# Performance work log

Hardware: AMD Instinct MI355X
Metric: run time of the kernel (lower is better)

Reference implementation:

```python
import jax, jax.numpy as jnp
import numpy as np

B, N, IN, HID, OUT, H = 8, 1024, 64, 64, 64, 4


def dense_gat(x, adj, W, a_src, a_dst, bias, heads):
    # x: [B,N,Fin], adj: [B,N,N] (0/1, self-loops already set), W: [heads*C, Fin]
    b, n, _ = x.shape
    c = W.shape[0] // heads
    h = (x @ W.T).reshape(b, n, heads, c)                      # [B,N,H,C]
    s = jnp.einsum('bnhc,hc->bnh', h, a_src)                   # source scores
    d = jnp.einsum('bnhc,hc->bnh', h, a_dst)                   # dest scores
    # alpha[b,i,j,h] = s[b,j,h] + d[b,i,h]
    alpha = s[:, None, :, :] + d[:, :, None, :]                # [B,N,N,H]
    alpha = jax.nn.leaky_relu(alpha, 0.2)
    alpha = jnp.where(adj[..., None] > 0, alpha, jnp.float32(-1e9))
    alpha = jax.nn.softmax(alpha, axis=2)                      # softmax over neighbors j
    out = jnp.einsum('bijh,bjhc->bihc', alpha, h)              # [B,N,H,C]
    return out.reshape(b, n, heads * c) + bias


def setup_inputs() -> dict:
    key = jax.random.key(0)
    ks = jax.random.split(key, 24)
    rn = lambda k, shape: (jax.random.normal(k, shape, jnp.float32) * 0.05)
    node_features = jax.random.normal(ks[0], (B, N, IN), jnp.float32)
    adj = jax.random.randint(ks[1], (B, N, N), 0, 2, jnp.int32)
    d = dict(
        node_features=node_features, adj=adj,
        w1=rn(ks[2], (H * HID, IN)),  as1=rn(ks[3], (H, HID)), ad1=rn(ks[4], (H, HID)), b1=rn(ks[5], (H * HID,)),
        w2=rn(ks[6], (H * HID, H * HID)), as2=rn(ks[7], (H, HID)), ad2=rn(ks[8], (H, HID)), b2=rn(ks[9], (H * HID,)),
        w3=rn(ks[10], (OUT, H * HID)), as3=rn(ks[11], (1, OUT)), ad3=rn(ks[12], (1, OUT)), b3=rn(ks[13], (OUT,)),
        wn=rn(ks[14], (OUT, OUT)), bn=rn(ks[15], (OUT,)),
        wg=rn(ks[16], (OUT, OUT)), bg=rn(ks[17], (OUT,)),
        wv=rn(ks[18], (1, 2 * OUT)), bv=rn(ks[19], (1,)),
    )
    return d


def reference(node_features, adj, w1, as1, ad1, b1, w2, as2, ad2, b2,
              w3, as3, ad3, b3, wn, bn, wg, bg, wv, bv):
    n = node_features.shape[1]
    adj_sl = jnp.maximum(adj, jnp.eye(n, dtype=adj.dtype)[None])  # add self-loops
    x = jax.nn.relu(dense_gat(node_features, adj_sl, w1, as1, ad1, b1, H))
    x = jax.nn.relu(dense_gat(x, adj_sl, w2, as2, ad2, b2, H))
    x = jax.nn.relu(dense_gat(x, adj_sl, w3, as3, ad3, b3, 1))     # [B,N,OUT]
    g = jnp.broadcast_to(x.sum(axis=-2, keepdims=True), x.shape)   # [B,N,OUT]
    h = jnp.concatenate([x @ wn.T + bn, g @ wg.T + bg], axis=-1)   # [B,N,2*OUT]
    h = jax.nn.relu(h)
    return (h @ wv.T + bv).squeeze(-1)                             # [B,N]
```

## Files before the change

kernel.cpp:

```cpp
#include <hip/hip_runtime.h>
#include <stdint.h>

#define NB 8
#define NN 1024
#define LOG2E 1.44269504088896f

typedef short short8 __attribute__((ext_vector_type(8)));
typedef float floatx4 __attribute__((ext_vector_type(4)));

static __device__ __forceinline__ short f2bf(float x) {
    union { float f; uint32_t u; } v; v.f = x;
    uint32_t r = (v.u + 0x7fffu + ((v.u >> 16) & 1u)) >> 16;
    return (short)r;
}

__global__ __launch_bounds__(256) void prep_all(const int* __restrict__ adj,
        uint64_t* __restrict__ am,
        const float* __restrict__ x0, const float* __restrict__ w1,
        const float* __restrict__ w2, const float* __restrict__ w3,
        const float* __restrict__ wn,
        ushort* __restrict__ x0b, ushort* __restrict__ wb1,
        ushort* __restrict__ wb2, ushort* __restrict__ wb3,
        ushort* __restrict__ wnb, float* __restrict__ gsum) {
    if (blockIdx.x < 2048) {
        int wave = blockIdx.x * 4 + (threadIdx.x >> 6);
        int lane = threadIdx.x & 63;
        int b = wave >> 10;
        int i = wave & 1023;
        const int* row = adj + ((size_t)b * NN + i) * NN;
        uint64_t* outp = am + ((size_t)b * NN + i) * 16;
        for (int it = 0; it < 16; ++it) {
            int j = it * 64 + lane;
            int v = (row[j] > 0) || (j == i);
            uint64_t m = __ballot(v);
            if (lane == 0) outp[it] = m;
        }
        return;
    }
    int idx = (blockIdx.x - 2048) * 256 + threadIdx.x;
    const float* src; ushort* dst; int li;
    if (idx < 131072)      { src = x0; dst = x0b; li = idx; }
    else if (idx < 135168) { src = w1; dst = wb1; li = idx - 131072; }
    else if (idx < 151552) { src = w2; dst = wb2; li = idx - 135168; }
    else if (idx < 155648) { src = w3; dst = wb3; li = idx - 151552; }
    else if (idx < 156672) { src = wn; dst = wnb; li = idx - 155648; }
    else if (idx < 156800) {
        ((float4*)gsum)[idx - 156672] = make_float4(0.f, 0.f, 0.f, 0.f);
        return;
    } else return;
    float4 v = ((const float4*)src)[li];
    ushort4 o;
    o.x = (ushort)f2bf(v.x); o.y = (ushort)f2bf(v.y);
    o.z = (ushort)f2bf(v.z); o.w = (ushort)f2bf(v.w);
    ((ushort4*)dst)[li] = o;
}

template<int K>
__global__ __launch_bounds__(256, 4) void gemm_mfma(const ushort* __restrict__ X,
        const ushort* __restrict__ Wt, ushort* __restrict__ hbT,
        const float* __restrict__ asrc, const float* __restrict__ adst,
        float* __restrict__ s_t, float* __restrict__ d_t, int nheads) {
    __shared__ ushort smem[2][64][88];
    int m0 = blockIdx.x * 64, n0 = blockIdx.y * 64;
    int hd = blockIdx.y;
    int tid = threadIdx.x, w = tid >> 6, L = tid & 63;
    int m15 = L & 15, kq = L >> 4;
    floatx4 acc[4];
#pragma unroll
    for (int ct = 0; ct < 4; ++ct) acc[ct] = (floatx4){0.f, 0.f, 0.f, 0.f};

    for (int k0 = 0; k0 < K; k0 += 64) {
#pragma unroll
        for (int it = 0; it < 2; ++it) {
            int idx = tid + it * 256;
            int r = idx >> 3, sg = idx & 7;
            *(uint4*)&smem[0][r][sg * 8] = *(const uint4*)&X[(size_t)(m0 + r) * K + k0 + sg * 8];
            *(uint4*)&smem[1][r][sg * 8] = *(const uint4*)&Wt[(size_t)(n0 + r) * K + k0 + sg * 8];
        }
        __syncthreads();
#pragma unroll
        for (int ks = 0; ks < 2; ++ks) {
            short8 a = *(const short8*)&smem[0][16 * w + m15][ks * 32 + kq * 8];
#pragma unroll
            for (int ct = 0; ct < 4; ++ct) {
                short8 bfr = *(const short8*)&smem[1][ct * 16 + m15][ks * 32 + kq * 8];
                acc[ct] = __builtin_amdgcn_mfma_f32_16x16x32_bf16(a, bfr, acc[ct], 0, 0, 0);
            }
        }
        __syncthreads();
    }

    float asv[4], adv[4];
#pragma unroll
    for (int ct = 0; ct < 4; ++ct) {
        asv[ct] = asrc[hd * 64 + ct * 16 + m15];
        adv[ct] = adst[hd * 64 + ct * 16 + m15];
    }
#pragma unroll
    for (int r = 0; r < 4; ++r) {
        float sp = acc[0][r] * asv[0] + acc[1][r] * asv[1] + acc[2][r] * asv[2] + acc[3][r] * asv[3];
        float dp = acc[0][r] * adv[0] + acc[1][r] * adv[1] + acc[2][r] * adv[2] + acc[3][r] * adv[3];
#pragma unroll
        for (int off = 1; off < 16; off <<= 1) {
            sp += __shfl_xor(sp, off);
            dp += __shfl_xor(dp, off);
        }
        if (m15 == 0) {
            int mg = m0 + 16 * w + kq * 4 + r;
            int bb = mg >> 10, node = mg & 1023;
            s_t[((size_t)(bb * nheads + hd)) * NN + node] = sp;
            d_t[((size_t)(bb * nheads + hd)) * NN + node] = dp;
        }
    }

    ushort* tb = (ushort*)smem;
#pragma unroll
    for (int ct = 0; ct < 4; ++ct)
#pragma unroll
        for (int r = 0; r < 4; ++r)
            tb[(ct * 16 + m15) * 80 + 16 * w + kq * 4 + r] = (ushort)f2bf(acc[ct][r]);
    __syncthreads();
    int bb = m0 >> 10, node0 = m0 & 1023;
    size_t base = ((size_t)(bb * nheads + hd) * 64) * NN + node0;
    int c = tid >> 2, s2 = (tid & 3) * 2;
#pragma unroll
    for (int e = 0; e < 2; ++e) {
        int sg = s2 + e;
        *(uint4*)&hbT[base + (size_t)c * NN + sg * 8] = *(const uint4*)&tb[c * 80 + sg * 8];
    }
}

__global__ __launch_bounds__(256, 4) void gat_agg_mfma(
        const ushort* __restrict__ hbT, const uint64_t* __restrict__ am,
        const float* __restrict__ s_t, const float* __restrict__ d_t,
        const float* __restrict__ bias, ushort* __restrict__ Xb,
        float* __restrict__ gsum, int nheads, int do_colsum) {
    __shared__ float s_lds[NN];
    __shared__ float d_lds[32];
    __shared__ float li_lds[32];
    __shared__ float red4[4];
    __shared__ float lsum_part[32];
    __shared__ uint64_t adj_lds[16][32];
    __shared__ ushort hb[2][64][88];

    int i0 = blockIdx.x * 32;
    int hd = blockIdx.y;
    int b  = blockIdx.z;
    int HC = nheads * 64;
    int tid = threadIdx.x, w = tid >> 6, L = tid & 63;
    int m15 = L & 15, kq = L >> 4;
    int p = w >> 1, q = w & 1;
    int tp = tid & 127;

    const float* srow = s_t + ((size_t)b * nheads + hd) * NN;
    const float* drow = d_t + ((size_t)b * nheads + hd) * NN;
    float lm = -1e30f;
    for (int j = tid; j < NN; j += 256) {
        float v = srow[j];
        s_lds[j] = v;
        lm = fmaxf(lm, v);
    }
#pragma unroll
    for (int off = 32; off; off >>= 1) lm = fmaxf(lm, __shfl_xor(lm, off));
    if (L == 0) red4[w] = lm;
    if (tid < 32) d_lds[tid] = drow[i0 + tid];
#pragma unroll
    for (int it = 0; it < 2; ++it) {
        int idx = tid + it * 256;
        int r = idx >> 4, wd = idx & 15;
        adj_lds[wd][r] = am[((size_t)b * NN + i0 + r) * 16 + wd];
    }
    __syncthreads();

    float smax = fmaxf(fmaxf(red4[0], red4[1]), fmaxf(red4[2], red4[3]));
    float d_i = d_lds[16 * q + m15];
    float m_up = smax + d_i;
    m_up = m_up > 0.f ? m_up : 0.2f * m_up;
    float m2n = -m_up * LOG2E;

    floatx4 acc[4];
#pragma unroll
    for (int ct = 0; ct < 4; ++ct) acc[ct] = (floatx4){0.f, 0.f, 0.f, 0.f};
    float lsum = 0.f;

    const ushort* hbase = hbT + ((size_t)(b * nheads + hd) * 64) * NN;

    for (int t = 0; t < 8; ++t) {
        int jc = p * 8 + t;
#pragma unroll
        for (int it = 0; it < 4; ++it) {
            int idx = tp + it * 128;
            int c = idx >> 3, sg = idx & 7;
            *(uint4*)&hb[p][c][sg * 8] = *(const uint4*)&hbase[(size_t)c * NN + jc * 64 + sg * 8];
        }
        __syncthreads();

        uint64_t word = adj_lds[jc][16 * q + m15];
#pragma unroll
        for (int ks = 0; ks < 2; ++ks) {
            int jb = jc * 64 + ks * 32 + kq * 8;
            float sv[8];
            *(float4*)&sv[0] = *(const float4*)&s_lds[jb];
            *(float4*)&sv[4] = *(const float4*)&s_lds[jb + 4];
            unsigned byte = (unsigned)((word >> (ks * 32 + kq * 8)) & 0xffull);
            short8 afrag;
#pragma unroll
            for (int u = 0; u < 8; ++u) {
                float sc = sv[u] + d_i;
                float lk = fmaxf(sc, 0.2f * sc);
#if __has_builtin(__builtin_amdgcn_exp2f)
                float arg = __builtin_fmaf(lk, LOG2E, m2n);
                arg = ((byte >> u) & 1u) ? arg : -1e30f;
                float e = __builtin_amdgcn_exp2f(arg);
#else
                float e = __expf(lk - m_up);
                e = ((byte >> u) & 1u) ? e : 0.f;
#endif
                lsum += e;
                ((ushort*)&afrag)[u] = (ushort)(__float_as_uint(e) >> 16);
            }
#pragma unroll
            for (int ct = 0; ct < 4; ++ct) {
                short8 bfr = *(const short8*)&hb[p][ct * 16 + m15][ks * 32 + kq * 8];
                acc[ct] = __builtin_amdgcn_mfma_f32_16x16x32_bf16(afrag, bfr, acc[ct], 0, 0, 0);
            }
        }
        __syncthreads();
    }

    lsum += __shfl_xor(lsum, 16);
    lsum += __shfl_xor(lsum, 32);

    float* accbuf = (float*)&hb[0][0][0];
    if (p == 1) {
#pragma unroll
        for (int ct = 0; ct < 4; ++ct)
#pragma unroll
            for (int r = 0; r < 4; ++r)
                accbuf[(16 * q + kq * 4 + r) * 66 + ct * 16 + m15] = acc[ct][r];
        if (kq == 0) lsum_part[16 * q + m15] = lsum;
    }
    __syncthreads();
    if (p == 0) {
#pragma unroll
        for (int ct = 0; ct < 4; ++ct)
#pragma unroll
            for (int r = 0; r < 4; ++r)
                acc[ct][r] += accbuf[(16 * q + kq * 4 + r) * 66 + ct * 16 + m15];
        float ltot = lsum + lsum_part[16 * q + m15];
        if (kq == 0) li_lds[16 * q + m15] = 1.f / ltot;
    }
    __syncthreads();

    if (p == 0) {
        float bv4[4];
#pragma unroll
        for (int ct = 0; ct < 4; ++ct) bv4[ct] = bias[hd * 64 + ct * 16 + m15];
#pragma unroll
        for (int ct = 0; ct < 4; ++ct) {
            float cs = 0.f;
#pragma unroll
            for (int r = 0; r < 4; ++r) {
                int row = 16 * q + kq * 4 + r;
                float v = acc[ct][r] * li_lds[row] + bv4[ct];
                v = fmaxf(v, 0.f);
                cs += v;
                size_t off = ((size_t)(b * NN + i0 + row)) * HC + hd * 64 + ct * 16 + m15;
                Xb[off] = (ushort)f2bf(v);
            }
            if (do_colsum) {
                cs += __shfl_xor(cs, 16);
                cs += __shfl_xor(cs, 32);
                if (kq == 0) atomicAdd(&gsum[b * 64 + ct * 16 + m15], cs);
            }
        }
    }
}

__global__ __launch_bounds__(256) void readout_fused(
        const ushort* __restrict__ xb, const ushort* __restrict__ wnb,
        const float* __restrict__ bn, const float* __restrict__ wg,
        const float* __restrict__ bg, const float* __restrict__ wv,
        const float* __restrict__ bv, const float* __restrict__ gsum,
        float* __restrict__ outp) {
    __shared__ ushort xs[64][88];
    __shared__ ushort wns[64][88];
    __shared__ float gcs;
    int b = blockIdx.y, n0 = blockIdx.x * 64;
    int tid = threadIdx.x, w = tid >> 6, L = tid & 63;
    int m15 = L & 15, kq = L >> 4;
#pragma unroll
    for (int it = 0; it < 2; ++it) {
        int idx = tid + it * 256;
        int r = idx >> 3, sg = idx & 7;
        *(uint4*)&xs[r][sg * 8]  = *(const uint4*)&xb[(size_t)(b * NN + n0 + r) * 64 + sg * 8];
        *(uint4*)&wns[r][sg * 8] = *(const uint4*)&wnb[r * 64 + sg * 8];
    }
    if (tid < 64) {
        float acc = bg[tid];
#pragma unroll 8
        for (int c = 0; c < 64; ++c) acc += gsum[b * 64 + c] * wg[tid * 64 + c];
        acc = fmaxf(acc, 0.f) * wv[64 + tid];
#pragma unroll
        for (int off = 32; off; off >>= 1) acc += __shfl_down(acc, off);
        if (tid == 0) gcs = acc + bv[0];
    }
    __syncthreads();

    floatx4 acc[4];
#pragma unroll
    for (int ct = 0; ct < 4; ++ct) acc[ct] = (floatx4){0.f, 0.f, 0.f, 0.f};
#pragma unroll
    for (int ks = 0; ks < 2; ++ks) {
        short8 a = *(const short8*)&xs[16 * w + m15][ks * 32 + kq * 8];
#pragma unroll
        for (int ct = 0; ct < 4; ++ct) {
            short8 bfr = *(const short8*)&wns[ct * 16 + m15][ks * 32 + kq * 8];
            acc[ct] = __builtin_amdgcn_mfma_f32_16x16x32_bf16(a, bfr, acc[ct], 0, 0, 0);
        }
    }
    float bnv[4], wvv[4];
#pragma unroll
    for (int ct = 0; ct < 4; ++ct) {
        bnv[ct] = bn[ct * 16 + m15];
        wvv[ct] = wv[ct * 16 + m15];
    }
    float gc = gcs;
#pragma unroll
    for (int r = 0; r < 4; ++r) {
        float rp = 0.f;
#pragma unroll
        for (int ct = 0; ct < 4; ++ct)
            rp += fmaxf(acc[ct][r] + bnv[ct], 0.f) * wvv[ct];
#pragma unroll
        for (int off = 1; off < 16; off <<= 1) rp += __shfl_xor(rp, off);
        if (m15 == 0)
            outp[(size_t)b * NN + n0 + 16 * w + kq * 4 + r] = rp + gc;
    }
}

extern "C" void kernel_launch(void* const* d_in, const int* in_sizes, int n_in,
                              void* d_out, int out_size, void* d_ws, size_t ws_size,
                              hipStream_t stream) {
    const float* x0  = (const float*)d_in[0];
    const int*   adj = (const int*)  d_in[1];
    const float* w1  = (const float*)d_in[2];
    const float* as1 = (const float*)d_in[3];
    const float* ad1 = (const float*)d_in[4];
    const float* b1  = (const float*)d_in[5];
    const float* w2  = (const float*)d_in[6];
    const float* as2 = (const float*)d_in[7];
    const float* ad2 = (const float*)d_in[8];
    const float* b2  = (const float*)d_in[9];
    const float* w3  = (const float*)d_in[10];
    const float* as3 = (const float*)d_in[11];
    const float* ad3 = (const float*)d_in[12];
    const float* b3  = (const float*)d_in[13];
    const float* wn  = (const float*)d_in[14];
    const float* bn  = (const float*)d_in[15];
    const float* wg  = (const float*)d_in[16];
    const float* bg  = (const float*)d_in[17];
    const float* wv  = (const float*)d_in[18];
    const float* bv  = (const float*)d_in[19];
    float* outp = (float*)d_out;

    char* wsb = (char*)d_ws;
    uint64_t* amask = (uint64_t*)(wsb);
    ushort* hbT  = (ushort*)(wsb + (1u  << 20));
    ushort* xbA  = (ushort*)(wsb + (5u  << 20));
    ushort* xbB  = (ushort*)(wsb + (9u  << 20));
    ushort* x0b  = (ushort*)(wsb + (13u << 20));
    char* tail   = wsb + (14u << 20);
    float* s_buf = (float*)(tail);
    float* d_buf = (float*)(tail + (1u << 17));
    ushort* wb1  = (ushort*)(tail + (2u << 17));
    ushort* wb2  = (ushort*)(tail + (2u << 17) + (1u << 15));
    ushort* wb3  = (ushort*)(tail + (2u << 17) + (5u << 15));
    ushort* wnb  = (ushort*)(tail + (2u << 17) + (6u << 15));
    float* gsum  = (float*) (tail + (2u << 17) + (6u << 15) + (1u << 13));

    prep_all<<<2661, 256, 0, stream>>>(adj, amask, x0, w1, w2, w3, wn,
                                       x0b, wb1, wb2, wb3, wnb, gsum);

    gemm_mfma<64><<<dim3(128, 4), 256, 0, stream>>>(x0b, wb1, hbT, as1, ad1, s_buf, d_buf, 4);
    gat_agg_mfma<<<dim3(32, 4, 8), 256, 0, stream>>>(hbT, amask, s_buf, d_buf, b1, xbA, gsum, 4, 0);

    gemm_mfma<256><<<dim3(128, 4), 256, 0, stream>>>(xbA, wb2, hbT, as2, ad2, s_buf, d_buf, 4);
    gat_agg_mfma<<<dim3(32, 4, 8), 256, 0, stream>>>(hbT, amask, s_buf, d_buf, b2, xbB, gsum, 4, 0);

    gemm_mfma<256><<<dim3(128, 1), 256, 0, stream>>>(xbB, wb3, hbT, as3, ad3, s_buf, d_buf, 1);
    gat_agg_mfma<<<dim3(32, 1, 8), 256, 0, stream>>>(hbT, amask, s_buf, d_buf, b3, xbA, gsum, 1, 1);

    readout_fused<<<dim3(16, 8), 256, 0, stream>>>(xbA, wnb, bn, wg, bg, wv, bv, gsum, outp);
}
```

Baseline: 208.4 us.

## Split GAT aggregation across four waves per 16-row tile with private LDS buffers

The aggregation kernel now handles 16 destination rows per block instead of 32, and each of the four waves processes a quarter of the neighbour range. Each wave stages its own h tile in a private, XOR-swizzled LDS buffer with register prefetch, which removes the per-chunk block-wide barriers. Partial accumulators and softmax denominators are reduced across waves through LDS at the end, with vectorised output stores and a block-level column sum before the atomics. The grid doubles, so there is more parallelism and less sync, at the cost of more redundant loads of s and of the h tiles across blocks.

```diff
diff --git a/kernel.cpp b/kernel.cpp
--- a/kernel.cpp
+++ b/kernel.cpp
@@ -136,46 +136,34 @@
         const float* __restrict__ bias, ushort* __restrict__ Xb,
         float* __restrict__ gsum, int nheads, int do_colsum) {
     __shared__ float s_lds[NN];
-    __shared__ float d_lds[32];
-    __shared__ float li_lds[32];
     __shared__ float red4[4];
-    __shared__ float lsum_part[32];
-    __shared__ uint64_t adj_lds[16][32];
-    __shared__ ushort hb[2][64][88];
-
-    int i0 = blockIdx.x * 32;
+    __shared__ ushort buf[4][4096];
+
+    int i0 = blockIdx.x * 16;
     int hd = blockIdx.y;
     int b  = blockIdx.z;
     int HC = nheads * 64;
     int tid = threadIdx.x, w = tid >> 6, L = tid & 63;
     int m15 = L & 15, kq = L >> 4;
-    int p = w >> 1, q = w & 1;
-    int tp = tid & 127;
 
     const float* srow = s_t + ((size_t)b * nheads + hd) * NN;
-    const float* drow = d_t + ((size_t)b * nheads + hd) * NN;
-    float lm = -1e30f;
-    for (int j = tid; j < NN; j += 256) {
-        float v = srow[j];
-        s_lds[j] = v;
-        lm = fmaxf(lm, v);
-    }
+    float4 s4 = ((const float4*)srow)[tid];
+    *(float4*)&s_lds[tid * 4] = s4;
+    float lm = fmaxf(fmaxf(s4.x, s4.y), fmaxf(s4.z, s4.w));
 #pragma unroll
     for (int off = 32; off; off >>= 1) lm = fmaxf(lm, __shfl_xor(lm, off));
     if (L == 0) red4[w] = lm;
-    if (tid < 32) d_lds[tid] = drow[i0 + tid];
-#pragma unroll
-    for (int it = 0; it < 2; ++it) {
-        int idx = tid + it * 256;
-        int r = idx >> 4, wd = idx & 15;
-        adj_lds[wd][r] = am[((size_t)b * NN + i0 + r) * 16 + wd];
-    }
+
+    const uint64_t* amrow = am + ((size_t)b * NN + i0 + m15) * 16 + w * 4;
+    uint64_t aw[4];
+    *(uint4*)&aw[0] = *(const uint4*)&amrow[0];
+    *(uint4*)&aw[2] = *(const uint4*)&amrow[2];
+    float d_i = d_t[((size_t)b * nheads + hd) * NN + i0 + m15];
     __syncthreads();
 
     float smax = fmaxf(fmaxf(red4[0], red4[1]), fmaxf(red4[2], red4[3]));
-    float d_i = d_lds[16 * q + m15];
-    float m_up = smax + d_i;
-    m_up = m_up > 0.f ? m_up : 0.2f * m_up;
+    float t0 = smax + d_i;
+    float m_up = fmaxf(t0, 0.2f * t0);
     float m2n = -m_up * LOG2E;
 
     floatx4 acc[4];
@@ -184,18 +172,26 @@
     float lsum = 0.f;
 
     const ushort* hbase = hbT + ((size_t)(b * nheads + hd) * 64) * NN;
-
-    for (int t = 0; t < 8; ++t) {
-        int jc = p * 8 + t;
-#pragma unroll
-        for (int it = 0; it < 4; ++it) {
-            int idx = tp + it * 128;
-            int c = idx >> 3, sg = idx & 7;
-            *(uint4*)&hb[p][c][sg * 8] = *(const uint4*)&hbase[(size_t)c * NN + jc * 64 + sg * 8];
-        }
-        __syncthreads();
-
-        uint64_t word = adj_lds[jc][16 * q + m15];
+    int r8 = L >> 3, sl = L & 7;
+    int wofs = r8 * 64 + ((sl ^ r8) * 8);
+    ushort* mybuf = buf[w];
+    const ushort* gsrc = hbase + (size_t)r8 * NN + (w * 4) * 64 + sl * 8;
+
+    uint4 pre[8];
+#pragma unroll
+    for (int e = 0; e < 8; ++e) pre[e] = *(const uint4*)(gsrc + (size_t)e * 8 * NN);
+
+#pragma unroll
+    for (int t = 0; t < 4; ++t) {
+        int jc = w * 4 + t;
+#pragma unroll
+        for (int e = 0; e < 8; ++e) *(uint4*)&mybuf[wofs + e * 512] = pre[e];
+        if (t < 3) {
+#pragma unroll
+            for (int e = 0; e < 8; ++e)
+                pre[e] = *(const uint4*)(gsrc + (size_t)e * 8 * NN + (t + 1) * 64);
+        }
+        uint64_t word = aw[t];
 #pragma unroll
         for (int ks = 0; ks < 2; ++ks) {
             int jb = jc * 64 + ks * 32 + kq * 8;
@@ -203,7 +199,7 @@
             *(float4*)&sv[0] = *(const float4*)&s_lds[jb];
             *(float4*)&sv[4] = *(const float4*)&s_lds[jb + 4];
             unsigned byte = (unsigned)((word >> (ks * 32 + kq * 8)) & 0xffull);
-            short8 afrag;
+            unsigned ue[8];
 #pragma unroll
             for (int u = 0; u < 8; ++u) {
                 float sc = sv[u] + d_i;
@@ -217,62 +213,69 @@
                 e = ((byte >> u) & 1u) ? e : 0.f;
 #endif
                 lsum += e;
-                ((ushort*)&afrag)[u] = (ushort)(__float_as_uint(e) >> 16);
+                ue[u] = __float_as_uint(e);
             }
+            unsigned pk[4];
+#pragma unroll
+            for (int k2 = 0; k2 < 4; ++k2)
+#if __has_builtin(__builtin_amdgcn_perm)
+                pk[k2] = __builtin_amdgcn_perm(ue[2 * k2 + 1], ue[2 * k2], 0x07060302u);
+#else
+                pk[k2] = (ue[2 * k2] >> 16) | (ue[2 * k2 + 1] & 0xffff0000u);
+#endif
+            short8 afrag;
+            *(uint4*)&afrag = *(uint4*)&pk[0];
+            int pslot = (ks * 4 + kq) ^ (m15 & 7);
 #pragma unroll
             for (int ct = 0; ct < 4; ++ct) {
-                short8 bfr = *(const short8*)&hb[p][ct * 16 + m15][ks * 32 + kq * 8];
+                short8 bfr = *(const short8*)&mybuf[(ct * 16 + m15) * 64 + pslot * 8];
                 acc[ct] = __builtin_amdgcn_mfma_f32_16x16x32_bf16(afrag, bfr, acc[ct], 0, 0, 0);
             }
         }
-        __syncthreads();
     }
 
     lsum += __shfl_xor(lsum, 16);
     lsum += __shfl_xor(lsum, 32);
 
-    float* accbuf = (float*)&hb[0][0][0];
-    if (p == 1) {
-#pragma unroll
-        for (int ct = 0; ct < 4; ++ct)
-#pragma unroll
-            for (int r = 0; r < 4; ++r)
-                accbuf[(16 * q + kq * 4 + r) * 66 + ct * 16 + m15] = acc[ct][r];
-        if (kq == 0) lsum_part[16 * q + m15] = lsum;
-    }
+    float* fb = (float*)&buf[w][0];
+#pragma unroll
+    for (int ct = 0; ct < 4; ++ct)
+#pragma unroll
+        for (int r = 0; r < 4; ++r)
+            fb[(kq * 4 + r) * 68 + ct * 16 + m15] = acc[ct][r];
+    if (kq == 0) fb[16 * 68 + m15] = lsum;
     __syncthreads();
-    if (p == 0) {
-#pragma unroll
-        for (int ct = 0; ct < 4; ++ct)
-#pragma unroll
-            for (int r = 0; r < 4; ++r)
-                acc[ct][r] += accbuf[(16 * q + kq * 4 + r) * 66 + ct * 16 + m15];
-        float ltot = lsum + lsum_part[16 * q + m15];
-        if (kq == 0) li_lds[16 * q + m15] = 1.f / ltot;
-    }
-    __syncthreads();
-
-    if (p == 0) {
-        float bv4[4];
-#pragma unroll
-        for (int ct = 0; ct < 4; ++ct) bv4[ct] = bias[hd * 64 + ct * 16 + m15];
-#pragma unroll
-        for (int ct = 0; ct < 4; ++ct) {
-            float cs = 0.f;
-#pragma unroll
-            for (int r = 0; r < 4; ++r) {
-                int row = 16 * q + kq * 4 + r;
-                float v = acc[ct][r] * li_lds[row] + bv4[ct];
-                v = fmaxf(v, 0.f);
-                cs += v;
-                size_t off = ((size_t)(b * NN + i0 + row)) * HC + hd * 64 + ct * 16 + m15;
-                Xb[off] = (ushort)f2bf(v);
-            }
-            if (do_colsum) {
-                cs += __shfl_xor(cs, 16);
-                cs += __shfl_xor(cs, 32);
-                if (kq == 0) atomicAdd(&gsum[b * 64 + ct * 16 + m15], cs);
-            }
+
+    int rr = tid >> 4, c0 = (tid & 15) * 4;
+    float s0 = 0.f, s1 = 0.f, s2 = 0.f, s3 = 0.f, ltot = 0.f;
+#pragma unroll
+    for (int w2 = 0; w2 < 4; ++w2) {
+        const float* f2 = (const float*)&buf[w2][0];
+        float4 a4 = *(const float4*)&f2[rr * 68 + c0];
+        s0 += a4.x; s1 += a4.y; s2 += a4.z; s3 += a4.w;
+        ltot += f2[16 * 68 + rr];
+    }
+    float li = 1.f / ltot;
+    float4 bv = *(const float4*)&bias[hd * 64 + c0];
+    float v0 = fmaxf(s0 * li + bv.x, 0.f);
+    float v1 = fmaxf(s1 * li + bv.y, 0.f);
+    float v2 = fmaxf(s2 * li + bv.z, 0.f);
+    float v3 = fmaxf(s3 * li + bv.w, 0.f);
+    ushort4 o;
+    o.x = (ushort)f2bf(v0); o.y = (ushort)f2bf(v1);
+    o.z = (ushort)f2bf(v2); o.w = (ushort)f2bf(v3);
+    *(ushort4*)&Xb[((size_t)(b * NN + i0 + rr)) * HC + hd * 64 + c0] = o;
+
+    if (do_colsum) {
+        __syncthreads();
+        float* cb = (float*)&buf[0][0];
+        *(float4*)&cb[rr * 68 + c0] = make_float4(v0, v1, v2, v3);
+        __syncthreads();
+        if (tid < 64) {
+            float s = 0.f;
+#pragma unroll
+            for (int r2 = 0; r2 < 16; ++r2) s += cb[r2 * 68 + tid];
+            atomicAdd(&gsum[b * 64 + tid], s);
         }
     }
 }
@@ -383,13 +386,13 @@
                                        x0b, wb1, wb2, wb3, wnb, gsum);
 
     gemm_mfma<64><<<dim3(128, 4), 256, 0, stream>>>(x0b, wb1, hbT, as1, ad1, s_buf, d_buf, 4);
-    gat_agg_mfma<<<dim3(32, 4, 8), 256, 0, stream>>>(hbT, amask, s_buf, d_buf, b1, xbA, gsum, 4, 0);
+    gat_agg_mfma<<<dim3(64, 4, 8), 256, 0, stream>>>(hbT, amask, s_buf, d_buf, b1, xbA, gsum, 4, 0);
 
     gemm_mfma<256><<<dim3(128, 4), 256, 0, stream>>>(xbA, wb2, hbT, as2, ad2, s_buf, d_buf, 4);
-    gat_agg_mfma<<<dim3(32, 4, 8), 256, 0, stream>>>(hbT, amask, s_buf, d_buf, b2, xbB, gsum, 4, 0);
+    gat_agg_mfma<<<dim3(64, 4, 8), 256, 0, stream>>>(hbT, amask, s_buf, d_buf, b2, xbB, gsum, 4, 0);
 
     gemm_mfma<256><<<dim3(128, 1), 256, 0, stream>>>(xbB, wb3, hbT, as3, ad3, s_buf, d_buf, 1);
-    gat_agg_mfma<<<dim3(32, 1, 8), 256, 0, stream>>>(hbT, amask, s_buf, d_buf, b3, xbA, gsum, 1, 1);
+    gat_agg_mfma<<<dim3(64, 1, 8), 256, 0, stream>>>(hbT, amask, s_buf, d_buf, b3, xbA, gsum, 1, 1);
 
     readout_fused<<<dim3(16, 8), 256, 0, stream>>>(xbA, wnb, bn, wg, bg, wv, bv, gsum, outp);
 }
```

Measured after the change: 183.3 us. 12.1% less time.
